# Performance work log

Measured on AMD Instinct MI355X. Metric: run time of the kernel, lower is better.

## Reference

```python
import jax, jax.numpy as jnp
import numpy as np

MAX_DISP = 4            # FunctionCorrelation hardwired max displacement
NEG_SLOPE = 0.1         # LeakyReLU negative slope from act_cfg


def setup_inputs() -> dict:
    key = jax.random.key(0)
    k1, k2 = jax.random.split(key)
    N, C, H, W = 8, 256, 80, 160
    feat1 = jax.random.normal(k1, (N, C, H, W), dtype=jnp.float32)
    feat2 = jax.random.normal(k2, (N, C, H, W), dtype=jnp.float32)
    return {"feat1": feat1, "feat2": feat2}


def _correlation(feat1, feat2):
    """PWC-Net windowed cross-correlation: 81 displacement channels,
    normalized by channel count C (as in FunctionCorrelation)."""
    N, C, H, W = feat1.shape
    D = 2 * MAX_DISP + 1  # 9
    f2p = jnp.pad(feat2, ((0, 0), (0, 0), (MAX_DISP, MAX_DISP), (MAX_DISP, MAX_DISP)))
    outs = []
    # fixed 9x9 displacement window; each iter reduces over C without
    # materializing the full [N, C, 81, H, W] tensor
    for dy in range(D):
        for dx in range(D):
            shifted = jax.lax.dynamic_slice(f2p, (0, 0, dy, dx), (N, C, H, W))
            outs.append(jnp.einsum('nchw,nchw->nhw', feat1, shifted))
    corr = jnp.stack(outs, axis=1) / jnp.asarray(C, feat1.dtype)  # [N, 81, H, W]
    return corr


def reference(feat1, feat2):
    # scaled=False -> scale_factor = 1.0; stride=1 so view is a no-op reshape
    corr = _correlation(feat1, feat2)
    return jax.nn.leaky_relu(corr, negative_slope=NEG_SLOPE)
```

## Files before the change

kernel.cpp:

```cpp
#include <hip/hip_runtime.h>
#include <stdint.h>


constexpr int MAXD = 4;
constexpr int N_ = 8, C_ = 256, H_ = 80, W_ = 160, HW_ = H_ * W_;
constexpr int YT = 8, XT = 8;
constexpr int KC = 32;
constexpr int NCH = C_ / KC;
constexpr int KLINE = 20;
constexpr int ROWW  = 16 * KLINE + 8;
constexpr int AW    = YT * ROWW;
constexpr int BWRD  = 16 * ROWW;
constexpr int BUFW  = AW + BWRD;
constexpr int NTHR  = 512;

typedef __attribute__((ext_vector_type(8))) short  frag_ab;
typedef __attribute__((ext_vector_type(4))) float  frag_cd;

__device__ __forceinline__ uint32_t pkbf(float a, float b) {
    uint32_t ua = __float_as_uint(a), ub = __float_as_uint(b);
    ua += 0x7fff + ((ua >> 16) & 1);
    ub += 0x7fff + ((ub >> 16) & 1);
    return (ua >> 16) | (ub & 0xffff0000u);
}

__global__ __launch_bounds__(NTHR, 4)
void corr_mfma_kernel(const float* __restrict__ f1,
                      const float* __restrict__ f2,
                      float* __restrict__ out)
{
    __shared__ uint32_t lds[2 * BUFW];

    const int t    = threadIdx.x;
    const int wy   = t >> 6;
    const int lane = t & 63;
    const int nn   = lane & 15;
    const int qq   = lane >> 4;

    const int bid = blockIdx.x;
    const int img = bid & 7;
    const int tr  = bid >> 3;
    const int y0  = (tr / 20) * YT;
    const int x0  = (tr % 20) * XT;
    const int phase = img;

    const float* f1n = f1 + (size_t)img * C_ * HW_;
    const float* f2n = f2 + (size_t)img * C_ * HW_;

    const int qB  = t & 3;
    const int cqB = (t >> 2) & 7;
    const int sB  = t >> 5;
    const int ysB = y0 + sB - MAXD;
    const bool rowokB = (unsigned)ysB < (unsigned)H_;
    const int xqB = x0 - MAXD + 4 * qB;
    const bool vB = rowokB && (xqB >= 0) && ((xqB + 3) < W_);
    const int offB = (4 * cqB) * HW_ + (rowokB ? ysB * W_ : 0) + (vB ? xqB : 0);
    const int bwrd = AW + sB * ROWW + (4 * qB) * KLINE + 2 * cqB;

    const int qA  = lane & 3;
    const int cqA = (lane >> 2) & 7;
    const int xA  = x0 + 4 * qA;
    const bool vA = (xA + 3) < W_;
    const int offA = (4 * cqA) * HW_ + (y0 + wy) * W_ + (vA ? xA : 0);
    const int awrd = wy * ROWW + (4 * qA) * KLINE + 2 * cqA;

    const int afrag_w    = wy * ROWW + nn * KLINE + 4 * qq;
    const int bfrag_base = AW + wy * ROWW + nn * KLINE + 4 * qq;

    frag_cd acc[9];
#pragma unroll
    for (int d = 0; d < 9; ++d) acc[d] = (frag_cd){0.f, 0.f, 0.f, 0.f};

    float4 ra[4], rb[4];

#define LOADS(c0)                                                             \
    {                                                                         \
        const int cb = (c0) * HW_;                                            \
        _Pragma("unroll")                                                     \
        for (int j = 0; j < 4; ++j)                                           \
            rb[j] = vB ? *(const float4*)(f2n + cb + offB + j * HW_)          \
                       : float4{0, 0, 0, 0};                                  \
        if (lane < 32) {                                                      \
            _Pragma("unroll")                                                 \
            for (int j = 0; j < 4; ++j)                                       \
                ra[j] = vA ? *(const float4*)(f1n + cb + offA + j * HW_)      \
                           : float4{0, 0, 0, 0};                              \
        }                                                                     \
    }

#define WRITES(buf)                                                           \
    {                                                                         \
        uint32_t* wp = lds + (buf) * BUFW;                                    \
        const float* b0 = (const float*)&rb[0];                               \
        const float* b1 = (const float*)&rb[1];                               \
        const float* b2 = (const float*)&rb[2];                               \
        const float* b3 = (const float*)&rb[3];                               \
        _Pragma("unroll")                                                     \
        for (int i = 0; i < 4; ++i) {                                         \
            uint2 w;                                                          \
            w.x = pkbf(b0[i], b1[i]);                                         \
            w.y = pkbf(b2[i], b3[i]);                                         \
            *(uint2*)(wp + bwrd + i * KLINE) = w;                             \
        }                                                                     \
        if (lane < 32) {                                                      \
            const float* a0 = (const float*)&ra[0];                           \
            const float* a1 = (const float*)&ra[1];                           \
            const float* a2 = (const float*)&ra[2];                           \
            const float* a3 = (const float*)&ra[3];                           \
            _Pragma("unroll")                                                 \
            for (int i = 0; i < 4; ++i) {                                     \
                uint2 w;                                                      \
                w.x = pkbf(a0[i], a1[i]);                                     \
                w.y = pkbf(a2[i], a3[i]);                                     \
                *(uint2*)(wp + awrd + i * KLINE) = w;                         \
            }                                                                 \
        }                                                                     \
    }

    LOADS(((phase) & 7) * KC);
    WRITES(0);
    __syncthreads();

    for (int i = 0; i < NCH; ++i) {
        const int p = i & 1;

        if (i + 1 < NCH) LOADS((((i + 1 + phase) & 7) * KC));

        const uint32_t* rp = lds + p * BUFW;
        const frag_ab af = *(const frag_ab*)(rp + afrag_w);
#pragma unroll
        for (int d = 0; d < 9; ++d) {
            const frag_ab bf = *(const frag_ab*)(rp + bfrag_base + d * ROWW);
            acc[d] = __builtin_amdgcn_mfma_f32_16x16x32_bf16(af, bf, acc[d], 0, 0, 0);
        }

        if (i + 1 < NCH) WRITES(1 - p);
        __syncthreads();
    }

    const float inv_c = 1.0f / (float)C_;
    const int y = y0 + wy;
#pragma unroll
    for (int d = 0; d < 9; ++d) {
#pragma unroll
        for (int r = 0; r < 4; ++r) {
            const int m  = 4 * qq + r;
            const int dx = nn - m;
            if (m < XT && (unsigned)dx <= 8u) {
                float e = acc[d][r] * inv_c;
                e = e > 0.0f ? e : 0.1f * e;
                const int ch = d * 9 + dx;
                out[((size_t)(img * 81 + ch) * H_ + y) * W_ + (x0 + m)] = e;
            }
        }
    }
}

extern "C" void kernel_launch(void* const* d_in, const int* in_sizes, int n_in,
                              void* d_out, int out_size, void* d_ws, size_t ws_size,
                              hipStream_t stream) {
    const float* f1 = (const float*)d_in[0];
    const float* f2 = (const float*)d_in[1];
    float* out = (float*)d_out;
    const int nblocks = N_ * (H_ / YT) * (W_ / XT);
    corr_mfma_kernel<<<dim3(nblocks), dim3(NTHR), 0, stream>>>(f1, f2, out);
}
```

Baseline: 305.8 us.

## Widen x tile to 16 pixels and use both MFMA rows per wave

The x tile grows from 8 to 16 output pixels, so each wave now fills all 16 rows of the MFMA A operand instead of half. Each wave issues two MFMAs per displacement row against overlapping 16-wide B windows, covering a 24-column halo. This halves the block count and cuts redundant halo loads of feat2 and wasted MFMA work per output. It costs more accumulator registers and a more complex load and store mapping. The second accumulator's results are partly discarded via masking.

```diff
diff --git a/kernel.cpp b/kernel.cpp
--- a/kernel.cpp
+++ b/kernel.cpp
@@ -4,14 +4,15 @@
 
 constexpr int MAXD = 4;
 constexpr int N_ = 8, C_ = 256, H_ = 80, W_ = 160, HW_ = H_ * W_;
-constexpr int YT = 8, XT = 8;
+constexpr int YT = 8, XT = 16;
 constexpr int KC = 32;
 constexpr int NCH = C_ / KC;
 constexpr int KLINE = 20;
-constexpr int ROWW  = 16 * KLINE + 8;
-constexpr int AW    = YT * ROWW;
-constexpr int BWRD  = 16 * ROWW;
-constexpr int BUFW  = AW + BWRD;
+constexpr int AROW  = 16 * KLINE;
+constexpr int BROW  = 24 * KLINE;
+constexpr int ASZ   = YT * AROW;
+constexpr int BSZ   = 16 * BROW;
+constexpr int BUFW  = ASZ + BSZ;
 constexpr int NTHR  = 512;
 
 typedef __attribute__((ext_vector_type(8))) short  frag_ab;
@@ -40,81 +41,91 @@
     const int bid = blockIdx.x;
     const int img = bid & 7;
     const int tr  = bid >> 3;
-    const int y0  = (tr / 20) * YT;
-    const int x0  = (tr % 20) * XT;
+    const int y0  = (tr / 10) * YT;
+    const int x0  = (tr % 10) * XT;
     const int phase = img;
 
     const float* f1n = f1 + (size_t)img * C_ * HW_;
     const float* f2n = f2 + (size_t)img * C_ * HW_;
 
-    const int qB  = t & 3;
+    const int xqB = t & 3;
     const int cqB = (t >> 2) & 7;
     const int sB  = t >> 5;
     const int ysB = y0 + sB - MAXD;
-    const bool rowokB = (unsigned)ysB < (unsigned)H_;
-    const int xqB = x0 - MAXD + 4 * qB;
-    const bool vB = rowokB && (xqB >= 0) && ((xqB + 3) < W_);
-    const int offB = (4 * cqB) * HW_ + (rowokB ? ysB * W_ : 0) + (vB ? xqB : 0);
-    const int bwrd = AW + sB * ROWW + (4 * qB) * KLINE + 2 * cqB;
+    const bool rokB = (unsigned)ysB < (unsigned)H_;
+    const int xB  = x0 - MAXD + 4 * xqB;
+    const bool vB1 = rokB && (xB >= 0);
+    const int offB1 = (4 * cqB) * HW_ + (rokB ? ysB * W_ : 0) + (vB1 ? xB : 0);
+    const int bwrd1 = ASZ + sB * BROW + (4 * xqB) * KLINE + 2 * cqB;
 
-    const int qA  = lane & 3;
-    const int cqA = (lane >> 2) & 7;
-    const int xA  = x0 + 4 * qA;
-    const bool vA = (xA + 3) < W_;
-    const int offA = (4 * cqA) * HW_ + (y0 + wy) * W_ + (vA ? xA : 0);
-    const int awrd = wy * ROWW + (4 * qA) * KLINE + 2 * cqA;
+    const int xq2 = 4 + (t & 1);
+    const int cp2 = (t >> 1) & 15;
+    const int s2  = t >> 5;
+    const int ys2 = y0 + s2 - MAXD;
+    const bool rok2 = (unsigned)ys2 < (unsigned)H_;
+    const int xB2 = x0 - MAXD + 4 * xq2;
+    const bool vB2 = rok2 && ((xB2 + 3) < W_);
+    const int offB2 = (2 * cp2) * HW_ + (rok2 ? ys2 * W_ : 0) + (vB2 ? xB2 : 0);
+    const int bwrd2 = ASZ + s2 * BROW + (4 * xq2) * KLINE + cp2;
 
-    const int afrag_w    = wy * ROWW + nn * KLINE + 4 * qq;
-    const int bfrag_base = AW + wy * ROWW + nn * KLINE + 4 * qq;
+    const int qA = t & 3;
+    const int pA = (t >> 2) & 15;
+    const int rA = t >> 6;
+    const int offA = (2 * pA) * HW_ + (y0 + rA) * W_ + (x0 + 4 * qA);
+    const int awrd = rA * AROW + (4 * qA) * KLINE + pA;
 
-    frag_cd acc[9];
+    const int afrag_w    = wy * AROW + nn * KLINE + 4 * qq;
+    const int bfrag_base = ASZ + wy * BROW + nn * KLINE + 4 * qq;
+
+    frag_cd acc[9][2];
 #pragma unroll
-    for (int d = 0; d < 9; ++d) acc[d] = (frag_cd){0.f, 0.f, 0.f, 0.f};
+    for (int d = 0; d < 9; ++d) {
+        acc[d][0] = (frag_cd){0.f, 0.f, 0.f, 0.f};
+        acc[d][1] = (frag_cd){0.f, 0.f, 0.f, 0.f};
+    }
 
-    float4 ra[4], rb[4];
+    float4 rb1[4], rb2[2], ra[2];
 
 #define LOADS(c0)                                                             \
     {                                                                         \
         const int cb = (c0) * HW_;                                            \
         _Pragma("unroll")                                                     \
         for (int j = 0; j < 4; ++j)                                           \
-            rb[j] = vB ? *(const float4*)(f2n + cb + offB + j * HW_)          \
-                       : float4{0, 0, 0, 0};                                  \
-        if (lane < 32) {                                                      \
-            _Pragma("unroll")                                                 \
-            for (int j = 0; j < 4; ++j)                                       \
-                ra[j] = vA ? *(const float4*)(f1n + cb + offA + j * HW_)      \
-                           : float4{0, 0, 0, 0};                              \
-        }                                                                     \
+            rb1[j] = vB1 ? *(const float4*)(f2n + cb + offB1 + j * HW_)       \
+                         : float4{0, 0, 0, 0};                                \
+        _Pragma("unroll")                                                     \
+        for (int j = 0; j < 2; ++j)                                           \
+            rb2[j] = vB2 ? *(const float4*)(f2n + cb + offB2 + j * HW_)       \
+                         : float4{0, 0, 0, 0};                                \
+        _Pragma("unroll")                                                     \
+        for (int j = 0; j < 2; ++j)                                           \
+            ra[j] = *(const float4*)(f1n + cb + offA + j * HW_);              \
     }
 
 #define WRITES(buf)                                                           \
     {                                                                         \
         uint32_t* wp = lds + (buf) * BUFW;                                    \
-        const float* b0 = (const float*)&rb[0];                               \
-        const float* b1 = (const float*)&rb[1];                               \
-        const float* b2 = (const float*)&rb[2];                               \
-        const float* b3 = (const float*)&rb[3];                               \
+        const float* b0 = (const float*)&rb1[0];                              \
+        const float* b1 = (const float*)&rb1[1];                              \
+        const float* b2 = (const float*)&rb1[2];                              \
+        const float* b3 = (const float*)&rb1[3];                              \
         _Pragma("unroll")                                                     \
         for (int i = 0; i < 4; ++i) {                                         \
             uint2 w;                                                          \
             w.x = pkbf(b0[i], b1[i]);                                         \
             w.y = pkbf(b2[i], b3[i]);                                         \
-            *(uint2*)(wp + bwrd + i * KLINE) = w;                             \
+            *(uint2*)(wp + bwrd1 + i * KLINE) = w;                            \
         }                                                                     \
-        if (lane < 32) {                                                      \
-            const float* a0 = (const float*)&ra[0];                           \
-            const float* a1 = (const float*)&ra[1];                           \
-            const float* a2 = (const float*)&ra[2];                           \
-            const float* a3 = (const float*)&ra[3];                           \
-            _Pragma("unroll")                                                 \
-            for (int i = 0; i < 4; ++i) {                                     \
-                uint2 w;                                                      \
-                w.x = pkbf(a0[i], a1[i]);                                     \
-                w.y = pkbf(a2[i], a3[i]);                                     \
-                *(uint2*)(wp + awrd + i * KLINE) = w;                         \
-            }                                                                 \
-        }                                                                     \
+        const float* e0 = (const float*)&rb2[0];                              \
+        const float* e1 = (const float*)&rb2[1];                              \
+        _Pragma("unroll")                                                     \
+        for (int i = 0; i < 4; ++i)                                           \
+            wp[bwrd2 + i * KLINE] = pkbf(e0[i], e1[i]);                       \
+        const float* a0 = (const float*)&ra[0];                               \
+        const float* a1 = (const float*)&ra[1];                               \
+        _Pragma("unroll")                                                     \
+        for (int i = 0; i < 4; ++i)                                           \
+            wp[awrd + i * KLINE] = pkbf(a0[i], a1[i]);                        \
     }
 
     LOADS(((phase) & 7) * KC);
@@ -130,8 +141,10 @@
         const frag_ab af = *(const frag_ab*)(rp + afrag_w);
 #pragma unroll
         for (int d = 0; d < 9; ++d) {
-            const frag_ab bf = *(const frag_ab*)(rp + bfrag_base + d * ROWW);
-            acc[d] = __builtin_amdgcn_mfma_f32_16x16x32_bf16(af, bf, acc[d], 0, 0, 0);
+            const frag_ab bf0 = *(const frag_ab*)(rp + bfrag_base + d * BROW);
+            acc[d][0] = __builtin_amdgcn_mfma_f32_16x16x32_bf16(af, bf0, acc[d][0], 0, 0, 0);
+            const frag_ab bf1 = *(const frag_ab*)(rp + bfrag_base + d * BROW + 8 * KLINE);
+            acc[d][1] = __builtin_amdgcn_mfma_f32_16x16x32_bf16(af, bf1, acc[d][1], 0, 0, 0);
         }
 
         if (i + 1 < NCH) WRITES(1 - p);
@@ -143,14 +156,18 @@
 #pragma unroll
     for (int d = 0; d < 9; ++d) {
 #pragma unroll
-        for (int r = 0; r < 4; ++r) {
-            const int m  = 4 * qq + r;
-            const int dx = nn - m;
-            if (m < XT && (unsigned)dx <= 8u) {
-                float e = acc[d][r] * inv_c;
-                e = e > 0.0f ? e : 0.1f * e;
-                const int ch = d * 9 + dx;
-                out[((size_t)(img * 81 + ch) * H_ + y) * W_ + (x0 + m)] = e;
+        for (int tl = 0; tl < 2; ++tl) {
+#pragma unroll
+            for (int r = 0; r < 4; ++r) {
+                const int m  = 4 * qq + r;
+                const int ng = nn + 8 * tl;
+                const int dx = ng - m;
+                if ((tl == 0 || ng >= 16) && (unsigned)dx <= 8u) {
+                    float e = acc[d][tl][r] * inv_c;
+                    e = e > 0.0f ? e : 0.1f * e;
+                    const int ch = d * 9 + dx;
+                    out[((size_t)(img * 81 + ch) * H_ + y) * W_ + (x0 + m)] = e;
+                }
             }
         }
     }
```

After: 278.4 us. 8.9% less time.

## Widen x tile to 16 with 1024-thread blocks and two-stage register prefetch

Applied to the files above, without the earlier changes.

Doubles the output tile width to 16 columns, so each MFMA uses all 16 A rows instead of 8, and splits the B window into two half-waves per row. Thread count rises to 1024 with specialized loader roles. Register prefetch now runs two chunks ahead using alternating register sets. The aim is less wasted MFMA work and less redundant halo loading, at the cost of higher register pressure and lower occupancy per block under launch_bounds(1024,4).

```diff
diff --git a/kernel.cpp b/kernel.cpp
--- a/kernel.cpp
+++ b/kernel.cpp
@@ -4,15 +4,16 @@
 
 constexpr int MAXD = 4;
 constexpr int N_ = 8, C_ = 256, H_ = 80, W_ = 160, HW_ = H_ * W_;
-constexpr int YT = 8, XT = 8;
+constexpr int YT = 8, XT = 16;
 constexpr int KC = 32;
 constexpr int NCH = C_ / KC;
 constexpr int KLINE = 20;
-constexpr int ROWW  = 16 * KLINE + 8;
-constexpr int AW    = YT * ROWW;
-constexpr int BWRD  = 16 * ROWW;
-constexpr int BUFW  = AW + BWRD;
-constexpr int NTHR  = 512;
+constexpr int AROW  = 16 * KLINE;
+constexpr int BROW  = 24 * KLINE;
+constexpr int ASZ   = YT * AROW;
+constexpr int BSZ   = 16 * BROW;
+constexpr int BUFW  = ASZ + BSZ;
+constexpr int NTHR  = 1024;
 
 typedef __attribute__((ext_vector_type(8))) short  frag_ab;
 typedef __attribute__((ext_vector_type(4))) float  frag_cd;
@@ -32,7 +33,9 @@
     __shared__ uint32_t lds[2 * BUFW];
 
     const int t    = threadIdx.x;
-    const int wy   = t >> 6;
+    const int wid  = t >> 6;
+    const int wy   = wid & 7;
+    const int h    = wid >> 3;
     const int lane = t & 63;
     const int nn   = lane & 15;
     const int qq   = lane >> 4;
@@ -40,101 +43,127 @@
     const int bid = blockIdx.x;
     const int img = bid & 7;
     const int tr  = bid >> 3;
-    const int y0  = (tr / 20) * YT;
-    const int x0  = (tr % 20) * XT;
+    const int y0  = (tr / 10) * YT;
+    const int x0  = (tr % 10) * XT;
     const int phase = img;
 
     const float* f1n = f1 + (size_t)img * C_ * HW_;
     const float* f2n = f2 + (size_t)img * C_ * HW_;
 
-    const int qB  = t & 3;
-    const int cqB = (t >> 2) & 7;
-    const int sB  = t >> 5;
-    const int ysB = y0 + sB - MAXD;
-    const bool rowokB = (unsigned)ysB < (unsigned)H_;
-    const int xqB = x0 - MAXD + 4 * qB;
-    const bool vB = rowokB && (xqB >= 0) && ((xqB + 3) < W_);
-    const int offB = (4 * cqB) * HW_ + (rowokB ? ysB * W_ : 0) + (vB ? xqB : 0);
-    const int bwrd = AW + sB * ROWW + (4 * qB) * KLINE + 2 * cqB;
+    const bool doB = (t < 768);
+    const bool isB1 = (t < 512);
+    const bool doA = (t >= 512);
 
-    const int qA  = lane & 3;
-    const int cqA = (lane >> 2) & 7;
-    const int xA  = x0 + 4 * qA;
-    const bool vA = (xA + 3) < W_;
-    const int offA = (4 * cqA) * HW_ + (y0 + wy) * W_ + (vA ? xA : 0);
-    const int awrd = wy * ROWW + (4 * qA) * KLINE + 2 * cqA;
+    const int xq1 = t & 3;
+    const int cq1 = (t >> 2) & 7;
+    const int s1  = t >> 5;
+    const int ys1 = y0 + s1 - MAXD;
+    const bool rok1 = (unsigned)ys1 < (unsigned)H_;
+    const int xB1 = x0 - MAXD + 4 * xq1;
+    const bool vB1 = rok1 && (xB1 >= 0);
+    const int offB1 = (4 * cq1) * HW_ + (rok1 ? ys1 * W_ : 0) + (vB1 ? xB1 : 0);
 
-    const int afrag_w    = wy * ROWW + nn * KLINE + 4 * qq;
-    const int bfrag_base = AW + wy * ROWW + nn * KLINE + 4 * qq;
+    const int u2  = (t >= 512) ? (t - 512) : 0;
+    const int xh2 = u2 & 1;
+    const int cq2 = (u2 >> 1) & 7;
+    const int s2  = u2 >> 4;
+    const int ys2 = y0 + s2 - MAXD;
+    const bool rok2 = (unsigned)ys2 < (unsigned)H_;
+    const int xB2 = x0 + 12 + 4 * xh2;
+    const bool vB2 = rok2 && ((xB2 + 3) < W_);
+    const int offB2 = (4 * cq2) * HW_ + (rok2 ? ys2 * W_ : 0) + (vB2 ? xB2 : 0);
+
+    const bool vB   = isB1 ? vB1 : vB2;
+    const int  offB = isB1 ? offB1 : offB2;
+    const int  bwrd = isB1 ? (ASZ + s1 * BROW + (4 * xq1) * KLINE + 2 * cq1)
+                           : (ASZ + s2 * BROW + (16 + 4 * xh2) * KLINE + 2 * cq2);
+
+    const int ua  = (t >= 512) ? (t - 512) : 0;
+    const int xqA = ua & 3;
+    const int cpA = (ua >> 2) & 15;
+    const int rA  = ua >> 6;
+    const int offA = (2 * cpA) * HW_ + (y0 + rA) * W_ + (x0 + 4 * xqA);
+    const int awrd = rA * AROW + (4 * xqA) * KLINE + cpA;
+
+    const int afrag = wy * AROW + nn * KLINE + 4 * qq;
+    const int bfrag = ASZ + wy * BROW + (8 * h + nn) * KLINE + 4 * qq;
 
     frag_cd acc[9];
 #pragma unroll
     for (int d = 0; d < 9; ++d) acc[d] = (frag_cd){0.f, 0.f, 0.f, 0.f};
 
-    float4 ra[4], rb[4];
+    float4 rb0[4], rb1[4], ra0[2], ra1[2];
 
-#define LOADS(c0)                                                             \
+#define CH(i) ((((i) + phase) & 7) * KC)
+
+#define LOADS(S, c0)                                                          \
     {                                                                         \
         const int cb = (c0) * HW_;                                            \
-        _Pragma("unroll")                                                     \
-        for (int j = 0; j < 4; ++j)                                           \
-            rb[j] = vB ? *(const float4*)(f2n + cb + offB + j * HW_)          \
-                       : float4{0, 0, 0, 0};                                  \
-        if (lane < 32) {                                                      \
+        if (doB) {                                                            \
             _Pragma("unroll")                                                 \
             for (int j = 0; j < 4; ++j)                                       \
-                ra[j] = vA ? *(const float4*)(f1n + cb + offA + j * HW_)      \
-                           : float4{0, 0, 0, 0};                              \
+                rb##S[j] = vB ? *(const float4*)(f2n + cb + offB + j * HW_)   \
+                              : float4{0, 0, 0, 0};                           \
+        }                                                                     \
+        if (doA) {                                                            \
+            _Pragma("unroll")                                                 \
+            for (int j = 0; j < 2; ++j)                                       \
+                ra##S[j] = *(const float4*)(f1n + cb + offA + j * HW_);       \
         }                                                                     \
     }
 
-#define WRITES(buf)                                                           \
+#define WRITES(buf, S)                                                        \
     {                                                                         \
         uint32_t* wp = lds + (buf) * BUFW;                                    \
-        const float* b0 = (const float*)&rb[0];                               \
-        const float* b1 = (const float*)&rb[1];                               \
-        const float* b2 = (const float*)&rb[2];                               \
-        const float* b3 = (const float*)&rb[3];                               \
-        _Pragma("unroll")                                                     \
-        for (int i = 0; i < 4; ++i) {                                         \
-            uint2 w;                                                          \
-            w.x = pkbf(b0[i], b1[i]);                                         \
-            w.y = pkbf(b2[i], b3[i]);                                         \
-            *(uint2*)(wp + bwrd + i * KLINE) = w;                             \
-        }                                                                     \
-        if (lane < 32) {                                                      \
-            const float* a0 = (const float*)&ra[0];                           \
-            const float* a1 = (const float*)&ra[1];                           \
-            const float* a2 = (const float*)&ra[2];                           \
-            const float* a3 = (const float*)&ra[3];                           \
+        if (doB) {                                                            \
+            const float* b0 = (const float*)&rb##S[0];                        \
+            const float* b1 = (const float*)&rb##S[1];                        \
+            const float* b2 = (const float*)&rb##S[2];                        \
+            const float* b3 = (const float*)&rb##S[3];                        \
             _Pragma("unroll")                                                 \
             for (int i = 0; i < 4; ++i) {                                     \
                 uint2 w;                                                      \
-                w.x = pkbf(a0[i], a1[i]);                                     \
-                w.y = pkbf(a2[i], a3[i]);                                     \
-                *(uint2*)(wp + awrd + i * KLINE) = w;                         \
+                w.x = pkbf(b0[i], b1[i]);                                     \
+                w.y = pkbf(b2[i], b3[i]);                                     \
+                *(uint2*)(wp + bwrd + i * KLINE) = w;                         \
             }                                                                 \
+        }                                                                     \
+        if (doA) {                                                            \
+            const float* a0 = (const float*)&ra##S[0];                        \
+            const float* a1 = (const float*)&ra##S[1];                        \
+            _Pragma("unroll")                                                 \
+            for (int i = 0; i < 4; ++i)                                       \
+                wp[awrd + i * KLINE] = pkbf(a0[i], a1[i]);                    \
         }                                                                     \
     }
 
-    LOADS(((phase) & 7) * KC);
-    WRITES(0);
+#define MFMAS(buf)                                                            \
+    {                                                                         \
+        const uint32_t* rp = lds + (buf) * BUFW;                              \
+        const frag_ab af = *(const frag_ab*)(rp + afrag);                     \
+        _Pragma("unroll")                                                     \
+        for (int d = 0; d < 9; ++d) {                                         \
+            const frag_ab bf = *(const frag_ab*)(rp + bfrag + d * BROW);      \
+            acc[d] = __builtin_amdgcn_mfma_f32_16x16x32_bf16(af, bf, acc[d],  \
+                                                             0, 0, 0);        \
+        }                                                                     \
+    }
+
+    LOADS(0, CH(0));
+    LOADS(1, CH(1));
+    WRITES(0, 0);
     __syncthreads();
 
-    for (int i = 0; i < NCH; ++i) {
-        const int p = i & 1;
+#pragma unroll 1
+    for (int i = 0; i < NCH; i += 2) {
+        if (i + 2 < NCH) LOADS(0, CH(i + 2));
+        MFMAS(0);
+        WRITES(1, 1);
+        __syncthreads();
 
-        if (i + 1 < NCH) LOADS((((i + 1 + phase) & 7) * KC));
-
-        const uint32_t* rp = lds + p * BUFW;
-        const frag_ab af = *(const frag_ab*)(rp + afrag_w);
-#pragma unroll
-        for (int d = 0; d < 9; ++d) {
-            const frag_ab bf = *(const frag_ab*)(rp + bfrag_base + d * ROWW);
-            acc[d] = __builtin_amdgcn_mfma_f32_16x16x32_bf16(af, bf, acc[d], 0, 0, 0);
-        }
-
-        if (i + 1 < NCH) WRITES(1 - p);
+        if (i + 3 < NCH) LOADS(1, CH(i + 3));
+        MFMAS(1);
+        if (i + 2 < NCH) WRITES(0, 0);
         __syncthreads();
     }
 
@@ -145,8 +174,9 @@
 #pragma unroll
         for (int r = 0; r < 4; ++r) {
             const int m  = 4 * qq + r;
-            const int dx = nn - m;
-            if (m < XT && (unsigned)dx <= 8u) {
+            const int j  = nn + 8 * h;
+            const int dx = j - m;
+            if ((h == 0 || nn >= 8) && (unsigned)dx <= 8u) {
                 float e = acc[d][r] * inv_c;
                 e = e > 0.0f ? e : 0.1f * e;
                 const int ch = d * 9 + dx;
```

After: 306.4 us. About the same (+0.2%).
